# Performance work log

Hardware: AMD Instinct MI355X
Metric: run time of the kernel (lower is better)

## Reference

```python
import jax, jax.numpy as jnp
import numpy as np

GRID_SIZE = 5
SPLINE_ORDER = 3
GRID_RANGE = (-1.0, 1.0)
LAYERS = [1024, 1024, 1024]
BATCH = 8192
LN_EPS = 1e-5


def _make_grid(in_features):
    h = (GRID_RANGE[1] - GRID_RANGE[0]) / GRID_SIZE
    n = GRID_SIZE + 2 * SPLINE_ORDER + 1  # 12 knots
    g = jnp.linspace(GRID_RANGE[0] - h * SPLINE_ORDER,
                     GRID_RANGE[1] + h * SPLINE_ORDER, n, dtype=jnp.float32)
    return jnp.broadcast_to(g, (in_features, n))


def setup_inputs() -> dict:
    key = jax.random.key(0)
    ks = jax.random.split(key, 8)
    n_layers = len(LAYERS) - 1
    d_in, d_out = LAYERS[0], LAYERS[1]  # square layers -> stackable params
    coeff = GRID_SIZE + SPLINE_ORDER  # 8
    # kaiming_uniform_(nonlinearity='linear'): bound = sqrt(3) * (1/sqrt(fan_in))
    bw_bound = float(np.sqrt(3.0) / np.sqrt(d_in))
    sw_bound = float(np.sqrt(3.0) / np.sqrt(d_in * coeff))
    x = jax.random.normal(ks[0], (BATCH, d_in), dtype=jnp.float32)
    base_w = jax.random.uniform(ks[1], (n_layers, d_out, d_in), jnp.float32, -bw_bound, bw_bound)
    spline_w = jax.random.uniform(ks[2], (n_layers, d_out, d_in, coeff), jnp.float32, -sw_bound, sw_bound)
    ln_g = jnp.ones((n_layers, d_out), jnp.float32)
    ln_b = jnp.zeros((n_layers, d_out), jnp.float32)
    prelu_a = jnp.full((n_layers,), 0.25, jnp.float32)
    grid = jnp.stack([_make_grid(d_in) for _ in range(n_layers)])  # [L, in, 12]
    return {"x": x, "base_w": base_w, "spline_w": spline_w,
            "ln_g": ln_g, "ln_b": ln_b, "prelu_a": prelu_a, "grid": grid}


def _bspline_bases(x, g):
    """Cox-de Boor recursion. x: [B, in], g: [in, n_knots] -> [B, in, G+order]."""
    xu = x[..., None]  # [B, in, 1]
    bases = ((xu >= g[:, :-1]) & (xu < g[:, 1:])).astype(x.dtype)  # [B, in, 11]
    for k in range(1, SPLINE_ORDER + 1):
        left = g[:, :-(k + 1)]
        right = g[:, k:-1]
        delta = jnp.where(right == left, jnp.ones_like(right), right - left)
        bases = ((xu - left) / delta * bases[..., :-1]
                 + (g[:, k + 1:] - xu) / (g[:, k + 1:] - g[:, 1:-k]) * bases[..., 1:])
    return bases  # [B, in, 8]


def kan_forward(x, base_w, spline_w, ln_g, ln_b, prelu_a, grid):
    n_layers = base_w.shape[0]
    for i in range(n_layers):
        base_out = jnp.matmul(jax.nn.gelu(x, approximate=False), base_w[i].T)  # [B, out]
        bases = _bspline_bases(x, grid[i])  # [B, in, 8]
        spline_out = jnp.matmul(bases.reshape(x.shape[0], -1),
                                spline_w[i].reshape(spline_w.shape[1], -1).T)  # [B, out]
        h = base_out + spline_out
        mu = jnp.mean(h, axis=-1, keepdims=True)
        var = jnp.var(h, axis=-1, keepdims=True)  # biased, matches torch LayerNorm
        h = (h - mu) * jax.lax.rsqrt(var + LN_EPS) * ln_g[i] + ln_b[i]
        x = jnp.where(h >= 0, h, prelu_a[i] * h)  # PReLU (scalar slope per layer)
    return x


def reference(x, base_w, spline_w, ln_g, ln_b, prelu_a, grid):
    return kan_forward(x, base_w, spline_w, ln_g, ln_b, prelu_a, grid)
```

## Files before the change

kernel.cpp:

```cpp
#include <hip/hip_runtime.h>
#include <hip/hip_bf16.h>
#include <cstdint>
#include <cstddef>

typedef __bf16 bf16_t;
typedef __bf16 bf16x8 __attribute__((ext_vector_type(8)));
typedef __bf16 bf16x4 __attribute__((ext_vector_type(4)));
typedef float  f32x4  __attribute__((ext_vector_type(4)));

#define DIM    1024
#define NCOEF  8
#define KTOT   (DIM + DIM * NCOEF)
#define NKNOT  12
#define BATCH  8192
#define LN_EPS 1e-5f

__device__ __forceinline__ float gelu_exact(float x) {
    return 0.5f * x * (1.0f + erff(x * 0.70710678118654752440f));
}

__device__ __forceinline__ void gl_lds16(const void* g, void* l) {
    __builtin_amdgcn_global_load_lds(
        (const __attribute__((address_space(1))) unsigned int*)(uintptr_t)g,
        (__attribute__((address_space(3))) unsigned int*)(uintptr_t)l, 16, 0, 0);
}

__device__ __forceinline__ uint64_t pack4bf(float a, float b, float c, float d) {
    union { bf16_t h[4]; uint64_t q; } u;
    u.h[0] = (bf16_t)a; u.h[1] = (bf16_t)b; u.h[2] = (bf16_t)c; u.h[3] = (bf16_t)d;
    return u.q;
}

__device__ __forceinline__ void spline8(float x, float g0, float invh,
                                        uint64_t& lo, uint64_t& hi) {
    float u = (x - g0) * invh;
    float jf = floorf(u);
    int j = (int)jf;
    float f = u - jf;
    float f2 = f * f, f3 = f2 * f;
    float om = 1.0f - f, om2 = om * om;
    float w0 = om2 * om * (1.0f / 6.0f);
    float w3 = f3 * (1.0f / 6.0f);
    float w1 = fmaf(0.5f, f3, 2.0f / 3.0f) - f2;
    float w2 = 1.0f - w0 - w1 - w3;
    uint64_t W64 = pack4bf(w0, w1, w2, w3);
    if (!(u >= 0.0f && u < 11.0f)) W64 = 0;
    int sh = (j - 3) * 16;
    if (sh >= 0) {
        int s = sh & 63;
        uint64_t loW = W64 << s;
        uint64_t hiW = s ? (W64 >> (64 - s)) : 0ull;
        lo = (sh < 64) ? loW : 0ull;
        hi = (sh < 64) ? hiW : loW;
    } else {
        lo = W64 >> (-sh);
        hi = 0ull;
    }
}

__global__ void pack_w(const float* __restrict__ bw, const float* __restrict__ sw,
                       bf16_t* __restrict__ W) {
    int idx = blockIdx.x * 256 + threadIdx.x;
    bf16_t* wrow = W + (size_t)(idx >> 10) * KTOT;
    int j = idx & 1023;
    wrow[j] = (bf16_t)bw[idx];
    const float4* sp = (const float4*)(sw + (size_t)idx * NCOEF);
    float4 s0 = sp[0], s1 = sp[1];
    bf16x8 v;
    v[0] = (bf16_t)s0.x; v[1] = (bf16_t)s0.y; v[2] = (bf16_t)s0.z; v[3] = (bf16_t)s0.w;
    v[4] = (bf16_t)s1.x; v[5] = (bf16_t)s1.y; v[6] = (bf16_t)s1.z; v[7] = (bf16_t)s1.w;
    *(bf16x8*)(wrow + DIM + j * NCOEF) = v;
}

__global__ void prep_A(const float* __restrict__ x, bf16_t* __restrict__ A,
                       const float* __restrict__ gp) {
    const int row = blockIdx.x, t = threadIdx.x;
    const float g0 = gp[0];
    const float invh = 1.0f / (gp[1] - gp[0]);
    f32x4 v = *(const f32x4*)(x + (size_t)row * DIM + t * 4);
    bf16_t* Ar = A + (size_t)row * KTOT;
    bf16x4 ge;
#pragma unroll
    for (int k = 0; k < 4; k++) ge[k] = (bf16_t)gelu_exact(v[k]);
    *(bf16x4*)(Ar + t * 4) = ge;
#pragma unroll
    for (int k = 0; k < 4; k++) {
        uint64_t lo, hi;
        union { uint64_t u[2]; uint4 q; } o;
        spline8(v[k], g0, invh, lo, hi);
        o.u[0] = lo; o.u[1] = hi;
        *(uint4*)(Ar + DIM + (t * 4 + k) * NCOEF) = o.q;
    }
}


#define STR2(x) #x
#define GATEV(N) asm volatile("s_waitcnt vmcnt(" STR2(N) ")" ::: "memory");

#define MF_ROW(I, A_) \
    acc[I][0] = __builtin_amdgcn_mfma_f32_16x16x32_bf16(A_, b0, acc[I][0], 0, 0, 0); \
    acc[I][1] = __builtin_amdgcn_mfma_f32_16x16x32_bf16(A_, b1, acc[I][1], 0, 0, 0); \
    acc[I][2] = __builtin_amdgcn_mfma_f32_16x16x32_bf16(A_, b2, acc[I][2], 0, 0, 0); \
    acc[I][3] = __builtin_amdgcn_mfma_f32_16x16x32_bf16(A_, b3, acc[I][3], 0, 0, 0);

#define TILE(T, S, SP, DOSTAGE, GATESTMT) { \
    bf16x8 a0, a1, a2, a3, a4, a5, a6, a7, b0, b1, b2, b3; \
     \
    { const bf16_t* Ab_ = ldsA + (S) * 8192 + aOff; \
      const bf16_t* Bb_ = ldsB + (S) * 8192 + bOff; \
      a0 = *(const bf16x8*)(Ab_);        a1 = *(const bf16x8*)(Ab_ + 512); \
      a2 = *(const bf16x8*)(Ab_ + 1024); a3 = *(const bf16x8*)(Ab_ + 1536); \
      b0 = *(const bf16x8*)(Bb_);        b1 = *(const bf16x8*)(Bb_ + 512); \
      b2 = *(const bf16x8*)(Bb_ + 1024); b3 = *(const bf16x8*)(Bb_ + 1536); } \
    if (DOSTAGE) { \
      gl_lds16(Ag0 + (size_t)((T) + 3) * 32, ldsA + (SP) * 8192 + tid * 8); \
      gl_lds16(Ag1 + (size_t)((T) + 3) * 32, ldsA + (SP) * 8192 + 4096 + tid * 8); } \
    __builtin_amdgcn_s_barrier(); \
    asm volatile("s_waitcnt lgkmcnt(0)" ::: "memory"); \
    __builtin_amdgcn_sched_barrier(0); \
    __builtin_amdgcn_s_setprio(1); \
    MF_ROW(0, a0) MF_ROW(1, a1) MF_ROW(2, a2) MF_ROW(3, a3) \
    __builtin_amdgcn_s_setprio(0); \
    __builtin_amdgcn_s_barrier(); \
     \
    { const bf16_t* Ab_ = ldsA + (S) * 8192 + aOff; \
      a4 = *(const bf16x8*)(Ab_ + 2048); a5 = *(const bf16x8*)(Ab_ + 2560); \
      a6 = *(const bf16x8*)(Ab_ + 3072); a7 = *(const bf16x8*)(Ab_ + 3584); } \
    if (DOSTAGE) { \
      gl_lds16(Bg0 + (size_t)((T) + 3) * 32, ldsB + (SP) * 8192 + tid * 8); \
      gl_lds16(Bg1 + (size_t)((T) + 3) * 32, ldsB + (SP) * 8192 + 4096 + tid * 8); } \
    GATESTMT \
    __builtin_amdgcn_s_barrier(); \
    asm volatile("s_waitcnt lgkmcnt(0)" ::: "memory"); \
    __builtin_amdgcn_sched_barrier(0); \
    __builtin_amdgcn_s_setprio(1); \
    MF_ROW(4, a4) MF_ROW(5, a5) MF_ROW(6, a6) MF_ROW(7, a7) \
    __builtin_amdgcn_s_setprio(0); \
    __builtin_amdgcn_s_barrier(); \
}

#define PSTAGE(T, S) \
    gl_lds16(Ag0 + (size_t)(T) * 32, ldsA + (S) * 8192 + tid * 8); \
    gl_lds16(Ag1 + (size_t)(T) * 32, ldsA + (S) * 8192 + 4096 + tid * 8); \
    gl_lds16(Bg0 + (size_t)(T) * 32, ldsB + (S) * 8192 + tid * 8); \
    gl_lds16(Bg1 + (size_t)(T) * 32, ldsB + (S) * 8192 + 4096 + tid * 8);

template<int NTK>
__global__ __launch_bounds__(512, 2) void gemm_ab(
    const bf16_t* __restrict__ A,
    const bf16_t* __restrict__ W,
    float* __restrict__ C,
    int mmask, int mshift, int rows) {
    __shared__ __align__(16) bf16_t lds[65536];
    bf16_t* __restrict__ ldsA = lds;
    bf16_t* __restrict__ ldsB = lds + 32768;

    const int tid = threadIdx.x;
    const int l = tid & 63, wv = tid >> 6;
    const int wm = wv >> 2, wn = wv & 3;

    const int chunk = gridDim.x >> 3;
    const int bid = blockIdx.x;
    const int wg = (bid & 7) * chunk + (bid >> 3);
    const int bm = wg & mmask;
    const int bn = (wg >> mshift) & 3;
    const int ks = wg >> (mshift + 2);
    const int row0 = bm << 8, col0 = bn << 8;
    const int koff0 = ks * (NTK * 32);

    const int srow = tid >> 2;
    const int slc = (tid & 3) ^ ((srow >> 1) & 3);
    const bf16_t* __restrict__ Ag0 = A + (size_t)(row0 + srow) * KTOT + koff0 + slc * 8;
    const bf16_t* __restrict__ Ag1 = Ag0 + (size_t)128 * KTOT;
    const bf16_t* __restrict__ Bg0 = W + (size_t)(col0 + srow) * KTOT + koff0 + slc * 8;
    const bf16_t* __restrict__ Bg1 = Bg0 + (size_t)128 * KTOT;

    const int l15 = l & 15;
    const int pc = (l >> 4) ^ ((l15 >> 1) & 3);
    const int aOff = (wm * 128 + l15) * 32 + pc * 8;
    const int bOff = (wn * 64 + l15) * 32 + pc * 8;

    f32x4 acc[8][4] = {};

    PSTAGE(0, 0)
    PSTAGE(1, 1)
    PSTAGE(2, 2)
    GATEV(8)
    __builtin_amdgcn_s_barrier();

#pragma unroll 1
    for (int t = 0; t < NTK - 4; t += 4) {
        TILE(t + 0, 0, 3, 1, GATEV(8))
        TILE(t + 1, 1, 0, 1, GATEV(8))
        TILE(t + 2, 2, 1, 1, GATEV(8))
        TILE(t + 3, 3, 2, 1, GATEV(8))
    }
    TILE(NTK - 4, 0, 3, 1, GATEV(8))
    TILE(NTK - 3, 1, 0, 0, GATEV(4))
    TILE(NTK - 2, 2, 0, 0, GATEV(0))
    TILE(NTK - 1, 3, 0, 0, ;)

    float* __restrict__ Cp = C + (size_t)ks * rows * DIM;
    const int r0 = row0 + wm * 128 + (l >> 4) * 4;
    const int c0 = col0 + wn * 64 + l15;
#pragma unroll
    for (int i = 0; i < 8; i++)
#pragma unroll
        for (int j = 0; j < 4; j++)
#pragma unroll
            for (int r = 0; r < 4; r++)
                Cp[(size_t)(r0 + i * 16 + r) * DIM + c0 + j * 16] = acc[i][j][r];
}

__global__ void ln_mid_A(const float* __restrict__ h, int rows, int ksplit,
                         const float* __restrict__ g_ln, const float* __restrict__ b_ln,
                         const float* __restrict__ pa, bf16_t* __restrict__ A,
                         const float* __restrict__ gp) {
    const int row = blockIdx.x, tid = threadIdx.x;
    const int w = tid >> 6, l = tid & 63;
    f32x4 v = {0.0f, 0.0f, 0.0f, 0.0f};
    for (int ks = 0; ks < ksplit; ks++)
        v += *(const f32x4*)(h + ((size_t)ks * rows + row) * DIM + tid * 4);
    float s = v[0] + v[1] + v[2] + v[3];
    float q = v[0] * v[0] + v[1] * v[1] + v[2] * v[2] + v[3] * v[3];
#pragma unroll
    for (int o = 32; o > 0; o >>= 1) { s += __shfl_xor(s, o); q += __shfl_xor(q, o); }
    __shared__ float rs[4], rq[4];
    if (l == 0) { rs[w] = s; rq[w] = q; }
    __syncthreads();
    s = rs[0] + rs[1] + rs[2] + rs[3];
    q = rq[0] + rq[1] + rq[2] + rq[3];
    float mean = s * (1.0f / DIM);
    float var = q * (1.0f / DIM) - mean * mean;
    float rstd = rsqrtf(var + LN_EPS);
    float a = pa[0];
    const float g0 = gp[0];
    const float invh = 1.0f / (gp[1] - gp[0]);
    bf16_t* Ar = A + (size_t)row * KTOT;
    bf16x4 ge;
#pragma unroll
    for (int c = 0; c < 4; c++) {
        int col = tid * 4 + c;
        float yv = (v[c] - mean) * rstd * g_ln[col] + b_ln[col];
        yv = (yv >= 0.0f) ? yv : a * yv;
        ge[c] = (bf16_t)gelu_exact(yv);
        uint64_t lo, hi;
        union { uint64_t u[2]; uint4 qv; } o;
        spline8(yv, g0, invh, lo, hi);
        o.u[0] = lo; o.u[1] = hi;
        *(uint4*)(Ar + DIM + (size_t)col * NCOEF) = o.qv;
    }
    *(bf16x4*)(Ar + tid * 4) = ge;
}

__global__ void ln_out(const float* __restrict__ h, int rows, int ksplit,
                       const float* __restrict__ g_ln, const float* __restrict__ b_ln,
                       const float* __restrict__ pa, float* __restrict__ out) {
    const int row = blockIdx.x, tid = threadIdx.x;
    const int w = tid >> 6, l = tid & 63;
    f32x4 v = {0.0f, 0.0f, 0.0f, 0.0f};
    for (int ks = 0; ks < ksplit; ks++)
        v += *(const f32x4*)(h + ((size_t)ks * rows + row) * DIM + tid * 4);
    float s = v[0] + v[1] + v[2] + v[3];
    float q = v[0] * v[0] + v[1] * v[1] + v[2] * v[2] + v[3] * v[3];
#pragma unroll
    for (int o = 32; o > 0; o >>= 1) { s += __shfl_xor(s, o); q += __shfl_xor(q, o); }
    __shared__ float rs[4], rq[4];
    if (l == 0) { rs[w] = s; rq[w] = q; }
    __syncthreads();
    s = rs[0] + rs[1] + rs[2] + rs[3];
    q = rq[0] + rq[1] + rq[2] + rq[3];
    float mean = s * (1.0f / DIM);
    float var = q * (1.0f / DIM) - mean * mean;
    float rstd = rsqrtf(var + LN_EPS);
    float a = pa[0];
    f32x4 o4;
#pragma unroll
    for (int c = 0; c < 4; c++) {
        int col = tid * 4 + c;
        float yv = (v[c] - mean) * rstd * g_ln[col] + b_ln[col];
        o4[c] = (yv >= 0.0f) ? yv : a * yv;
    }
    *(f32x4*)(out + (size_t)row * DIM + tid * 4) = o4;
}

extern "C" void kernel_launch(void* const* d_in, const int* in_sizes, int n_in,
                              void* d_out, int out_size, void* d_ws, size_t ws_size,
                              hipStream_t stream) {
    const float* x    = (const float*)d_in[0];
    const float* bw   = (const float*)d_in[1];
    const float* sw   = (const float*)d_in[2];
    const float* ln_g = (const float*)d_in[3];
    const float* ln_b = (const float*)d_in[4];
    const float* pa   = (const float*)d_in[5];
    const float* gridK = (const float*)d_in[6];
    float* out = (float*)d_out;

    const size_t wbytes = (size_t)2 * DIM * KTOT * sizeof(bf16_t);
    int R = 8192, ksplit = 2;
    for (;;) {
        size_t need = wbytes + (size_t)R * KTOT * 2 + (size_t)ksplit * R * DIM * 4;
        if (need <= ws_size || R == 512) break;
        R >>= 1;
        int mt = R / 256;
        ksplit = (mt >= 32) ? 2 : (mt >= 16) ? 4 : 8;
    }
    int mtiles = R / 256;
    int mshift = 0; while ((1 << mshift) < mtiles) mshift++;
    int mmask = mtiles - 1;
    int grid = mtiles * 4 * ksplit;

    char* wsc = (char*)d_ws;
    bf16_t* Wbuf = (bf16_t*)wsc;
    bf16_t* Abuf = (bf16_t*)(wsc + wbytes);
    float*  hbuf = (float*)(wsc + wbytes + (size_t)R * KTOT * 2);

    pack_w<<<(2 * DIM * DIM) / 256, 256, 0, stream>>>(bw, sw, Wbuf);

    auto launch_gemm = [&](const bf16_t* Wl, hipStream_t st) {
        if (ksplit == 2)
            gemm_ab<144><<<grid, 512, 0, st>>>(Abuf, Wl, hbuf, mmask, mshift, R);
        else if (ksplit == 4)
            gemm_ab<72><<<grid, 512, 0, st>>>(Abuf, Wl, hbuf, mmask, mshift, R);
        else
            gemm_ab<36><<<grid, 512, 0, st>>>(Abuf, Wl, hbuf, mmask, mshift, R);
    };

    const int nslab = BATCH / R;
    for (int sidx = 0; sidx < nslab; sidx++) {
        const size_t row0 = (size_t)sidx * R;
        const float* x0 = x + row0 * DIM;
        prep_A<<<R, 256, 0, stream>>>(x0, Abuf, gridK);
        launch_gemm(Wbuf, stream);
        ln_mid_A<<<R, 256, 0, stream>>>(hbuf, R, ksplit, ln_g, ln_b, pa,
                                        Abuf, gridK + DIM * NKNOT);
        launch_gemm(Wbuf + (size_t)DIM * KTOT, stream);
        ln_out<<<R, 256, 0, stream>>>(hbuf, R, ksplit, ln_g + DIM, ln_b + DIM,
                                      pa + 1, out + row0 * DIM);
    }
}
```

Before: 566.2 us.

## Prefetch next tile's LDS fragments into registers during current MFMA phase

```diff
diff --git a/kernel.cpp b/kernel.cpp
--- a/kernel.cpp
+++ b/kernel.cpp
@@ -96,6 +96,8 @@
 
 #define STR2(x) #x
 #define GATEV(N) asm volatile("s_waitcnt vmcnt(" STR2(N) ")" ::: "memory");
+#define LGKM(N)  asm volatile("s_waitcnt lgkmcnt(" STR2(N) ")" ::: "memory");
+#define BAR() { __builtin_amdgcn_s_barrier(); asm volatile("" ::: "memory"); }
 
 #define MF_ROW(I, A_) \
     acc[I][0] = __builtin_amdgcn_mfma_f32_16x16x32_bf16(A_, b0, acc[I][0], 0, 0, 0); \
@@ -103,40 +105,42 @@
     acc[I][2] = __builtin_amdgcn_mfma_f32_16x16x32_bf16(A_, b2, acc[I][2], 0, 0, 0); \
     acc[I][3] = __builtin_amdgcn_mfma_f32_16x16x32_bf16(A_, b3, acc[I][3], 0, 0, 0);
 
-#define TILE(T, S, SP, DOSTAGE, GATESTMT) { \
-    bf16x8 a0, a1, a2, a3, a4, a5, a6, a7, b0, b1, b2, b3; \
+#define TILE(T, S, SN, SP, DOSTAGE, GATESTMT, DOEARLY, WAITB) { \
      \
-    { const bf16_t* Ab_ = ldsA + (S) * 8192 + aOff; \
-      const bf16_t* Bb_ = ldsB + (S) * 8192 + bOff; \
-      a0 = *(const bf16x8*)(Ab_);        a1 = *(const bf16x8*)(Ab_ + 512); \
-      a2 = *(const bf16x8*)(Ab_ + 1024); a3 = *(const bf16x8*)(Ab_ + 1536); \
-      b0 = *(const bf16x8*)(Bb_);        b1 = *(const bf16x8*)(Bb_ + 512); \
-      b2 = *(const bf16x8*)(Bb_ + 1024); b3 = *(const bf16x8*)(Bb_ + 1536); } \
     if (DOSTAGE) { \
       gl_lds16(Ag0 + (size_t)((T) + 3) * 32, ldsA + (SP) * 8192 + tid * 8); \
       gl_lds16(Ag1 + (size_t)((T) + 3) * 32, ldsA + (SP) * 8192 + 4096 + tid * 8); } \
-    __builtin_amdgcn_s_barrier(); \
-    asm volatile("s_waitcnt lgkmcnt(0)" ::: "memory"); \
+    BAR() \
+    { const bf16_t* Ab_ = ldsA + (S) * 8192 + aOff; \
+      a4 = *(const bf16x8*)(Ab_ + 2048); a5 = *(const bf16x8*)(Ab_ + 2560); \
+      a6 = *(const bf16x8*)(Ab_ + 3072); a7 = *(const bf16x8*)(Ab_ + 3584); } \
+    LGKM(4) \
     __builtin_amdgcn_sched_barrier(0); \
     __builtin_amdgcn_s_setprio(1); \
     MF_ROW(0, a0) MF_ROW(1, a1) MF_ROW(2, a2) MF_ROW(3, a3) \
     __builtin_amdgcn_s_setprio(0); \
-    __builtin_amdgcn_s_barrier(); \
+    BAR() \
      \
-    { const bf16_t* Ab_ = ldsA + (S) * 8192 + aOff; \
-      a4 = *(const bf16x8*)(Ab_ + 2048); a5 = *(const bf16x8*)(Ab_ + 2560); \
-      a6 = *(const bf16x8*)(Ab_ + 3072); a7 = *(const bf16x8*)(Ab_ + 3584); } \
     if (DOSTAGE) { \
       gl_lds16(Bg0 + (size_t)((T) + 3) * 32, ldsB + (SP) * 8192 + tid * 8); \
       gl_lds16(Bg1 + (size_t)((T) + 3) * 32, ldsB + (SP) * 8192 + 4096 + tid * 8); } \
     GATESTMT \
-    __builtin_amdgcn_s_barrier(); \
-    asm volatile("s_waitcnt lgkmcnt(0)" ::: "memory"); \
+    BAR() \
+    if (DOEARLY) { \
+      const bf16_t* An_ = ldsA + (SN) * 8192 + aOff; \
+      const bf16_t* Bn_ = ldsB + (SN) * 8192 + bOff; \
+      na0 = *(const bf16x8*)(An_);        na1 = *(const bf16x8*)(An_ + 512); \
+      na2 = *(const bf16x8*)(An_ + 1024); na3 = *(const bf16x8*)(An_ + 1536); \
+      nb0 = *(const bf16x8*)(Bn_);        nb1 = *(const bf16x8*)(Bn_ + 512); \
+      nb2 = *(const bf16x8*)(Bn_ + 1024); nb3 = *(const bf16x8*)(Bn_ + 1536); } \
+    WAITB \
     __builtin_amdgcn_sched_barrier(0); \
     __builtin_amdgcn_s_setprio(1); \
     MF_ROW(4, a4) MF_ROW(5, a5) MF_ROW(6, a6) MF_ROW(7, a7) \
     __builtin_amdgcn_s_setprio(0); \
-    __builtin_amdgcn_s_barrier(); \
+    BAR() \
+    a0 = na0; a1 = na1; a2 = na2; a3 = na3; \
+    b0 = nb0; b1 = nb1; b2 = nb2; b3 = nb3; \
 }
 
 #define PSTAGE(T, S) \
@@ -181,24 +185,34 @@
     const int bOff = (wn * 64 + l15) * 32 + pc * 8;
 
     f32x4 acc[8][4] = {};
+    bf16x8 a0, a1, a2, a3, a4, a5, a6, a7, b0, b1, b2, b3;
+    bf16x8 na0, na1, na2, na3, nb0, nb1, nb2, nb3;
 
     PSTAGE(0, 0)
     PSTAGE(1, 1)
     PSTAGE(2, 2)
     GATEV(8)
-    __builtin_amdgcn_s_barrier();
+    BAR()
+    {
+        const bf16_t* An_ = ldsA + aOff;
+        const bf16_t* Bn_ = ldsB + bOff;
+        a0 = *(const bf16x8*)(An_);        a1 = *(const bf16x8*)(An_ + 512);
+        a2 = *(const bf16x8*)(An_ + 1024); a3 = *(const bf16x8*)(An_ + 1536);
+        b0 = *(const bf16x8*)(Bn_);        b1 = *(const bf16x8*)(Bn_ + 512);
+        b2 = *(const bf16x8*)(Bn_ + 1024); b3 = *(const bf16x8*)(Bn_ + 1536);
+    }
 
 #pragma unroll 1
     for (int t = 0; t < NTK - 4; t += 4) {
-        TILE(t + 0, 0, 3, 1, GATEV(8))
-        TILE(t + 1, 1, 0, 1, GATEV(8))
-        TILE(t + 2, 2, 1, 1, GATEV(8))
-        TILE(t + 3, 3, 2, 1, GATEV(8))
-    }
-    TILE(NTK - 4, 0, 3, 1, GATEV(8))
-    TILE(NTK - 3, 1, 0, 0, GATEV(4))
-    TILE(NTK - 2, 2, 0, 0, GATEV(0))
-    TILE(NTK - 1, 3, 0, 0, ;)
+        TILE(t + 0, 0, 1, 3, 1, GATEV(8), 1, LGKM(8))
+        TILE(t + 1, 1, 2, 0, 1, GATEV(8), 1, LGKM(8))
+        TILE(t + 2, 2, 3, 1, 1, GATEV(8), 1, LGKM(8))
+        TILE(t + 3, 3, 0, 2, 1, GATEV(8), 1, LGKM(8))
+    }
+    TILE(NTK - 4, 0, 1, 3, 1, GATEV(8), 1, LGKM(8))
+    TILE(NTK - 3, 1, 2, 0, 0, GATEV(4), 1, LGKM(8))
+    TILE(NTK - 2, 2, 3, 1, 0, GATEV(0), 1, LGKM(8))
+    TILE(NTK - 1, 3, 0, 2, 0, ;,        0, LGKM(0))
 
     float* __restrict__ Cp = C + (size_t)ks * rows * DIM;
     const int r0 = row0 + wm * 128 + (l >> 4) * 4;
```

After: 568.2 us. Within noise of the previous version (+0.3%).
